# Kernel tuning notes

Hardware: AMD Instinct MI355X
Metric: run time of the kernel (lower is better)

The kernel has to match this reference:

```python
import jax, jax.numpy as jnp
import numpy as np
from jax.scipy.special import logsumexp

ITERS = 50
EPS = 0.005
B, N, D = 8, 2048, 3


def _sq_cost(x, y):
    x2 = jnp.sum(x * x, axis=-1)  # [B,N]
    y2 = jnp.sum(y * y, axis=-1)  # [B,M]
    c = x2[:, :, None] + y2[:, None, :] - 2.0 * jnp.einsum('bnd,bmd->bnm', x, y)
    return jnp.maximum(c, 0.0)


def setup_inputs() -> dict:
    key = jax.random.key(0)
    k1, k2 = jax.random.split(key)
    input1 = jax.random.normal(k1, (B, N, D), dtype=jnp.float32)
    input2 = jax.random.normal(k2, (B, N, D), dtype=jnp.float32)
    return {"input1": input1, "input2": input2}


def reference(input1, input2):
    # Approximate EMD between equal-size point sets, as in emdModule(x, y, eps, iters):
    # iterative entropic-regularized (Sinkhorn/auction-style) assignment on the
    # squared-distance cost, eps = entropic temperature, iters = sweeps.
    eps = jnp.float32(EPS)
    b, n, _ = input1.shape
    m = input2.shape[1]
    C = _sq_cost(input1, input2)  # [B,N,M]
    log_mu = -jnp.log(jnp.float32(n))
    log_nu = -jnp.log(jnp.float32(m))

    def body(carry, _):
        f, g = carry  # duals [B,N], [B,M]
        f = eps * (log_mu - logsumexp((g[:, None, :] - C) / eps, axis=2))
        g = eps * (log_nu - logsumexp((f[:, :, None] - C) / eps, axis=1))
        return (f, g), None

    f0 = jnp.zeros((b, n), dtype=C.dtype)
    g0 = jnp.zeros((b, m), dtype=C.dtype)
    (f, g), _ = jax.lax.scan(body, (f0, g0), None, length=ITERS)

    # transport plan; each row sums to 1/N (soft assignment)
    P = jnp.exp((f[:, :, None] + g[:, None, :] - C) / eps)  # [B,N,M]
    # per-point assigned squared distance (dis of emdModule), then .mean()
    dis = jnp.sum(P * C, axis=-1) * jnp.float32(n)  # [B,N]
    return jnp.mean(dis)
```

## Files before the change

kernel.cpp:

```cpp
#include <hip/hip_runtime.h>
#include <math.h>

#define NB 8
#define NN 2048
#define NM 2048
#define NITERS 50

static constexpr float F_EPS  = 0.005f;
static constexpr float LOG2E  = 1.4426950408889634f;
static constexpr float KK     = LOG2E / F_EPS;
static constexpr float TWOK   = 2.0f * KK;
static constexpr float NEG_LOG2N = -11.0f;

__device__ __forceinline__ float fexp2(float x) { return __builtin_amdgcn_exp2f(x); }
__device__ __forceinline__ float flog2(float x) { return __builtin_amdgcn_logf(x); }

__global__ void pack_init(const float* __restrict__ V, float4* __restrict__ Pout, int total)
{
    int i = blockIdx.x * blockDim.x + threadIdx.x;
    if (i < total) {
        float v0 = V[3*i], v1 = V[3*i+1], v2 = V[3*i+2];
        float s  = fmaf(v0, v0, fmaf(v1, v1, v2*v2));
        Pout[i]  = make_float4(v0, v1, v2, -KK * s);
    }
}

__global__ __launch_bounds__(256, 4) void sink_update(
    const float4* __restrict__ Pin,
    const float*  __restrict__ Vraw,
    float4*       __restrict__ Pout)
{
    __shared__ float2 part [16][257];
    __shared__ float2 part2[16][17];
    const int tid  = threadIdx.x;
    const int lane = tid & 63;
    const int wave = tid >> 6;
    const int wgs_per_b = NN / 16;
    const int b       = blockIdx.x / wgs_per_b;
    const int rowbase = (blockIdx.x % wgs_per_b) * 16;

    float xs0[16], xs1[16], xs2[16];
    {
        const float* vb = Vraw + ((size_t)(b * NN + rowbase)) * 3;
        #pragma unroll
        for (int r = 0; r < 16; ++r) {
            xs0[r] = TWOK * vb[r*3+0];
            xs1[r] = TWOK * vb[r*3+1];
            xs2[r] = TWOK * vb[r*3+2];
        }
    }

    const float4* __restrict__ pp = Pin + b * NM + wave * 512 + lane;

    float rm[16], rs[16];
    #pragma unroll
    for (int r = 0; r < 16; ++r) { rm[r] = -1e30f; rs[r] = 0.f; }

    #pragma unroll
    for (int ib = 0; ib < 2; ++ib) {
        const float4 c0 = pp[(ib*4 + 0) * 64];
        const float4 c1 = pp[(ib*4 + 1) * 64];
        const float4 c2 = pp[(ib*4 + 2) * 64];
        const float4 c3 = pp[(ib*4 + 3) * 64];
        #pragma unroll
        for (int r = 0; r < 16; ++r) {
            const float z0 = fmaf(xs0[r], c0.x, fmaf(xs1[r], c0.y, fmaf(xs2[r], c0.z, c0.w)));
            const float z1 = fmaf(xs0[r], c1.x, fmaf(xs1[r], c1.y, fmaf(xs2[r], c1.z, c1.w)));
            const float z2 = fmaf(xs0[r], c2.x, fmaf(xs1[r], c2.y, fmaf(xs2[r], c2.z, c2.w)));
            const float z3 = fmaf(xs0[r], c3.x, fmaf(xs1[r], c3.y, fmaf(xs2[r], c3.z, c3.w)));
            const float cm = fmaxf(fmaxf(z0, z1), fmaxf(z2, z3));
            const float nm = fmaxf(rm[r], cm);
            const float s  = (fexp2(z0 - nm) + fexp2(z1 - nm))
                           + (fexp2(z2 - nm) + fexp2(z3 - nm));
            rs[r] = fmaf(rs[r], fexp2(rm[r] - nm), s);
            rm[r] = nm;
        }
    }

    #pragma unroll
    for (int r = 0; r < 16; ++r)
        part[r][tid] = make_float2(rm[r], rs[r]);
    __syncthreads();

    {
        const int row = tid & 15, seg = tid >> 4;
        float m16 = -1e30f;
        float2 v[16];
        #pragma unroll
        for (int k = 0; k < 16; ++k) { v[k] = part[row][seg*16 + k]; m16 = fmaxf(m16, v[k].x); }
        float s16 = 0.f;
        #pragma unroll
        for (int k = 0; k < 16; ++k) s16 = fmaf(v[k].y, fexp2(v[k].x - m16), s16);
        part2[row][seg] = make_float2(m16, s16);
    }
    __syncthreads();

    if (tid < 16) {
        float gm = -1e30f;
        float2 v[16];
        #pragma unroll
        for (int k = 0; k < 16; ++k) { v[k] = part2[tid][k]; gm = fmaxf(gm, v[k].x); }
        float s = 0.f;
        #pragma unroll
        for (int k = 0; k < 16; ++k) s = fmaf(v[k].y, fexp2(v[k].x - gm), s);
        const float lse2 = gm + flog2(s);
        const int n0 = rowbase + tid;
        const float* vp = Vraw + ((size_t)(b * NN + n0)) * 3;
        Pout[b * NN + n0] = make_float4(vp[0], vp[1], vp[2], NEG_LOG2N - lse2);
    }
}

__global__ __launch_bounds__(256, 4) void final_loss(
    const float4* __restrict__ Px, const float4* __restrict__ Py,
    float* __restrict__ out)
{
    __shared__ float wsum[4];
    const int tid  = threadIdx.x;
    const int lane = tid & 63;
    const int wave = tid >> 6;
    const int wgs_per_b = NN / 16;
    const int b       = blockIdx.x / wgs_per_b;
    const int rowbase = (blockIdx.x % wgs_per_b) * 16;

    float xr0[16], xr1[16], xr2[16], Af[16], xq[16];
    {
        const float4* xb = Px + b * NN + rowbase;
        #pragma unroll
        for (int r = 0; r < 16; ++r) {
            const float4 xp = xb[r];
            xr0[r] = xp.x; xr1[r] = xp.y; xr2[r] = xp.z; Af[r] = xp.w;
            xq[r]  = fmaf(xp.x, xp.x, fmaf(xp.y, xp.y, xp.z * xp.z));
        }
    }

    const float4* __restrict__ pp = Py + b * NM + wave * 512 + lane;

    float acc = 0.f;
    #pragma unroll
    for (int i = 0; i < 8; ++i) {
        const float4 p = pp[i * 64];
        const float ysq = fmaf(p.x, p.x, fmaf(p.y, p.y, p.z * p.z));
        #pragma unroll
        for (int r = 0; r < 16; ++r) {
            const float dot = fmaf(xr0[r], p.x, fmaf(xr1[r], p.y, xr2[r] * p.z));
            const float cc  = fmaxf(fmaf(-2.f, dot, xq[r] + ysq), 0.f);
            const float zp  = fmaf(TWOK, dot, Af[r] + p.w);
            acc = fmaf(fexp2(zp), cc, acc);
        }
    }
    #pragma unroll
    for (int o = 32; o > 0; o >>= 1) acc += __shfl_xor(acc, o);
    if (lane == 0) wsum[wave] = acc;
    __syncthreads();
    if (tid == 0) {
        atomicAdd(out, (wsum[0] + wsum[1] + wsum[2] + wsum[3]) * (1.0f / NB));
    }
}

extern "C" void kernel_launch(void* const* d_in, const int* in_sizes, int n_in,
                              void* d_out, int out_size, void* d_ws, size_t ws_size,
                              hipStream_t stream)
{
    const float* x = (const float*)d_in[0];
    const float* y = (const float*)d_in[1];
    float4* Px = (float4*)d_ws;
    float4* Py = Px + NB * NN;

    pack_init<<<(NB * NM + 255) / 256, 256, 0, stream>>>(y, Py, NB * NM);

    for (int it = 0; it < NITERS; ++it) {
        sink_update<<<NB * NN / 16, 256, 0, stream>>>(Py, x, Px);
        sink_update<<<NB * NM / 16, 256, 0, stream>>>(Px, y, Py);
    }

    hipMemsetAsync(d_out, 0, sizeof(float), stream);
    final_loss<<<NB * NN / 16, 256, 0, stream>>>(Px, Py, (float*)d_out);
}
```

Baseline: 1.121 ms.

## Use SoA layout, two-pass max-then-sum logsumexp with wave-skip, packed FMA

Converts the point and dual storage from AoS float4 to SoA arrays so each lane loads four consecutive columns with vector loads and uses packed 2-wide FMAs. The online logsumexp becomes two passes: first the row max, then exp-sums. A wave-uniform skip bypasses exp work when every lane's values are more than 28 log2 units below the max. The final loss likewise skips terms whose exponent is below -40. It also interleaves batches across blocks. The costs are recomputing the dot products twice and a small approximation from the skipped tiny terms.

Result: slower. 2.406 ms (+114.6%).

```diff
diff --git a/kernel.cpp b/kernel.cpp
--- a/kernel.cpp
+++ b/kernel.cpp
@@ -6,80 +6,130 @@
 #define NM 2048
 #define NITERS 50
 
-static constexpr float F_EPS  = 0.005f;
 static constexpr float LOG2E  = 1.4426950408889634f;
-static constexpr float KK     = LOG2E / F_EPS;
+static constexpr float KK     = LOG2E / 0.005f;
 static constexpr float TWOK   = 2.0f * KK;
 static constexpr float NEG_LOG2N = -11.0f;
+static constexpr float SKIP   = 28.0f;
+static constexpr float ZP_CUT = -40.0f;
+
+typedef float v2f __attribute__((ext_vector_type(2)));
 
 __device__ __forceinline__ float fexp2(float x) { return __builtin_amdgcn_exp2f(x); }
 __device__ __forceinline__ float flog2(float x) { return __builtin_amdgcn_logf(x); }
-
-__global__ void pack_init(const float* __restrict__ V, float4* __restrict__ Pout, int total)
+__device__ __forceinline__ v2f fma2(float s, v2f a, v2f b) {
+    return __builtin_elementwise_fma((v2f){s, s}, a, b);
+}
+__device__ __forceinline__ v2f vfma2(v2f a, v2f b, v2f c) {
+    return __builtin_elementwise_fma(a, b, c);
+}
+__device__ __forceinline__ v2f max2(v2f a, v2f b) { return __builtin_elementwise_max(a, b); }
+
+__global__ void pack_soa(const float* __restrict__ X, const float* __restrict__ Y,
+                         float* __restrict__ Xx, float* __restrict__ Xy, float* __restrict__ Xz,
+                         float* __restrict__ Yx, float* __restrict__ Yy, float* __restrict__ Yz,
+                         float* __restrict__ SwY)
 {
     int i = blockIdx.x * blockDim.x + threadIdx.x;
-    if (i < total) {
-        float v0 = V[3*i], v1 = V[3*i+1], v2 = V[3*i+2];
-        float s  = fmaf(v0, v0, fmaf(v1, v1, v2*v2));
-        Pout[i]  = make_float4(v0, v1, v2, -KK * s);
+    if (i < NB * NN) {
+        float a = X[3*i], b = X[3*i+1], c = X[3*i+2];
+        Xx[i] = a; Xy[i] = b; Xz[i] = c;
+        float d = Y[3*i], e = Y[3*i+1], f = Y[3*i+2];
+        Yx[i] = d; Yy[i] = e; Yz[i] = f;
+        SwY[i] = -KK * fmaf(d, d, fmaf(e, e, f * f));
     }
 }
 
 __global__ __launch_bounds__(256, 4) void sink_update(
-    const float4* __restrict__ Pin,
-    const float*  __restrict__ Vraw,
-    float4*       __restrict__ Pout)
+    const float* __restrict__ Ux, const float* __restrict__ Uy,
+    const float* __restrict__ Uz, const float* __restrict__ Uw,
+    const float* __restrict__ Ox, const float* __restrict__ Oy,
+    const float* __restrict__ Oz,
+    float* __restrict__ SwOut)
 {
     __shared__ float2 part [16][257];
     __shared__ float2 part2[16][17];
     const int tid  = threadIdx.x;
     const int lane = tid & 63;
     const int wave = tid >> 6;
-    const int wgs_per_b = NN / 16;
-    const int b       = blockIdx.x / wgs_per_b;
-    const int rowbase = (blockIdx.x % wgs_per_b) * 16;
+    const int b    = blockIdx.x & 7;
+    const int wgb  = blockIdx.x >> 3;
+    const int rowbase = wgb * 16;
 
     float xs0[16], xs1[16], xs2[16];
-    {
-        const float* vb = Vraw + ((size_t)(b * NN + rowbase)) * 3;
+    #pragma unroll
+    for (int r = 0; r < 16; ++r) {
+        const int n = b * NN + rowbase + r;
+        xs0[r] = TWOK * Ox[n]; xs1[r] = TWOK * Oy[n]; xs2[r] = TWOK * Oz[n];
+    }
+
+    const int m0 = b * NM + wave * 512 + lane * 4;
+
+    float rm[16];
+    #pragma unroll
+    for (int r = 0; r < 16; ++r) rm[r] = -1e30f;
+
+    #pragma unroll
+    for (int c = 0; c < 2; ++c) {
+        const int mo = m0 + c * 256;
+        const float4 vx = *(const float4*)(Ux + mo);
+        const float4 vy = *(const float4*)(Uy + mo);
+        const float4 vz = *(const float4*)(Uz + mo);
+        const float4 vw = *(const float4*)(Uw + mo);
+        const v2f xlo = {vx.x, vx.y}, xhi = {vx.z, vx.w};
+        const v2f ylo = {vy.x, vy.y}, yhi = {vy.z, vy.w};
+        const v2f zlo = {vz.x, vz.y}, zhi = {vz.z, vz.w};
+        const v2f wlo = {vw.x, vw.y}, whi = {vw.z, vw.w};
         #pragma unroll
         for (int r = 0; r < 16; ++r) {
-            xs0[r] = TWOK * vb[r*3+0];
-            xs1[r] = TWOK * vb[r*3+1];
-            xs2[r] = TWOK * vb[r*3+2];
+            v2f za = fma2(xs0[r], xlo, wlo);
+            za     = fma2(xs1[r], ylo, za);
+            za     = fma2(xs2[r], zlo, za);
+            v2f zb = fma2(xs0[r], xhi, whi);
+            zb     = fma2(xs1[r], yhi, zb);
+            zb     = fma2(xs2[r], zhi, zb);
+            const v2f mm = max2(za, zb);
+            rm[r] = fmaxf(rm[r], fmaxf(mm.x, mm.y));
         }
     }
 
-    const float4* __restrict__ pp = Pin + b * NM + wave * 512 + lane;
-
-    float rm[16], rs[16];
-    #pragma unroll
-    for (int r = 0; r < 16; ++r) { rm[r] = -1e30f; rs[r] = 0.f; }
-
-    #pragma unroll
-    for (int ib = 0; ib < 2; ++ib) {
-        const float4 c0 = pp[(ib*4 + 0) * 64];
-        const float4 c1 = pp[(ib*4 + 1) * 64];
-        const float4 c2 = pp[(ib*4 + 2) * 64];
-        const float4 c3 = pp[(ib*4 + 3) * 64];
+    float rs[16];
+    #pragma unroll
+    for (int r = 0; r < 16; ++r) rs[r] = 0.f;
+
+    #pragma unroll
+    for (int c = 0; c < 2; ++c) {
+        const int mo = m0 + c * 256;
+        const float4 vx = *(const float4*)(Ux + mo);
+        const float4 vy = *(const float4*)(Uy + mo);
+        const float4 vz = *(const float4*)(Uz + mo);
+        const float4 vw = *(const float4*)(Uw + mo);
+        const v2f xlo = {vx.x, vx.y}, xhi = {vx.z, vx.w};
+        const v2f ylo = {vy.x, vy.y}, yhi = {vy.z, vy.w};
+        const v2f zlo = {vz.x, vz.y}, zhi = {vz.z, vz.w};
+        const v2f wlo = {vw.x, vw.y}, whi = {vw.z, vw.w};
         #pragma unroll
         for (int r = 0; r < 16; ++r) {
-            const float z0 = fmaf(xs0[r], c0.x, fmaf(xs1[r], c0.y, fmaf(xs2[r], c0.z, c0.w)));
-            const float z1 = fmaf(xs0[r], c1.x, fmaf(xs1[r], c1.y, fmaf(xs2[r], c1.z, c1.w)));
-            const float z2 = fmaf(xs0[r], c2.x, fmaf(xs1[r], c2.y, fmaf(xs2[r], c2.z, c2.w)));
-            const float z3 = fmaf(xs0[r], c3.x, fmaf(xs1[r], c3.y, fmaf(xs2[r], c3.z, c3.w)));
-            const float cm = fmaxf(fmaxf(z0, z1), fmaxf(z2, z3));
-            const float nm = fmaxf(rm[r], cm);
-            const float s  = (fexp2(z0 - nm) + fexp2(z1 - nm))
-                           + (fexp2(z2 - nm) + fexp2(z3 - nm));
-            rs[r] = fmaf(rs[r], fexp2(rm[r] - nm), s);
-            rm[r] = nm;
+            v2f za = fma2(xs0[r], xlo, wlo);
+            za     = fma2(xs1[r], ylo, za);
+            za     = fma2(xs2[r], zlo, za);
+            v2f zb = fma2(xs0[r], xhi, whi);
+            zb     = fma2(xs1[r], yhi, zb);
+            zb     = fma2(xs2[r], zhi, zb);
+            const v2f mm = max2(za, zb);
+            const float cm = fmaxf(mm.x, mm.y);
+            if (__any(cm > rm[r] - SKIP)) {
+                const float e0 = fexp2(za.x - rm[r]);
+                const float e1 = fexp2(za.y - rm[r]);
+                const float e2 = fexp2(zb.x - rm[r]);
+                const float e3 = fexp2(zb.y - rm[r]);
+                rs[r] += (e0 + e1) + (e2 + e3);
+            }
         }
     }
 
     #pragma unroll
-    for (int r = 0; r < 16; ++r)
-        part[r][tid] = make_float2(rm[r], rs[r]);
+    for (int r = 0; r < 16; ++r) part[r][tid] = make_float2(rm[r], rs[r]);
     __syncthreads();
 
     {
@@ -104,57 +154,77 @@
         #pragma unroll
         for (int k = 0; k < 16; ++k) s = fmaf(v[k].y, fexp2(v[k].x - gm), s);
         const float lse2 = gm + flog2(s);
-        const int n0 = rowbase + tid;
-        const float* vp = Vraw + ((size_t)(b * NN + n0)) * 3;
-        Pout[b * NN + n0] = make_float4(vp[0], vp[1], vp[2], NEG_LOG2N - lse2);
+        SwOut[b * NN + rowbase + tid] = NEG_LOG2N - lse2;
     }
 }
 
 __global__ __launch_bounds__(256, 4) void final_loss(
-    const float4* __restrict__ Px, const float4* __restrict__ Py,
+    const float* __restrict__ Xx, const float* __restrict__ Xy,
+    const float* __restrict__ Xz, const float* __restrict__ SwX,
+    const float* __restrict__ Yx, const float* __restrict__ Yy,
+    const float* __restrict__ Yz, const float* __restrict__ SwY,
     float* __restrict__ out)
 {
     __shared__ float wsum[4];
     const int tid  = threadIdx.x;
     const int lane = tid & 63;
     const int wave = tid >> 6;
-    const int wgs_per_b = NN / 16;
-    const int b       = blockIdx.x / wgs_per_b;
-    const int rowbase = (blockIdx.x % wgs_per_b) * 16;
-
-    float xr0[16], xr1[16], xr2[16], Af[16], xq[16];
-    {
-        const float4* xb = Px + b * NN + rowbase;
+    const int b    = blockIdx.x & 7;
+    const int wgb  = blockIdx.x >> 3;
+    const int rowbase = wgb * 16;
+
+    float px[16], py[16], pz[16], Af[16], xq[16];
+    #pragma unroll
+    for (int r = 0; r < 16; ++r) {
+        const int n = b * NN + rowbase + r;
+        px[r] = Xx[n]; py[r] = Xy[n]; pz[r] = Xz[n];
+        Af[r] = SwX[n];
+        xq[r] = fmaf(px[r], px[r], fmaf(py[r], py[r], pz[r] * pz[r]));
+    }
+
+    const int m0 = b * NM + wave * 512 + lane * 4;
+
+    float acc = 0.f;
+    #pragma unroll
+    for (int c = 0; c < 2; ++c) {
+        const int mo = m0 + c * 256;
+        const float4 vx = *(const float4*)(Yx + mo);
+        const float4 vy = *(const float4*)(Yy + mo);
+        const float4 vz = *(const float4*)(Yz + mo);
+        const float4 vw = *(const float4*)(SwY + mo);
+        const v2f xlo = {vx.x, vx.y}, xhi = {vx.z, vx.w};
+        const v2f ylo = {vy.x, vy.y}, yhi = {vy.z, vy.w};
+        const v2f zlo = {vz.x, vz.y}, zhi = {vz.z, vz.w};
+        const v2f wlo = {vw.x, vw.y}, whi = {vw.z, vw.w};
+        const v2f yqlo = vfma2(xlo, xlo, vfma2(ylo, ylo, zlo * zlo));
+        const v2f yqhi = vfma2(xhi, xhi, vfma2(yhi, yhi, zhi * zhi));
         #pragma unroll
         for (int r = 0; r < 16; ++r) {
-            const float4 xp = xb[r];
-            xr0[r] = xp.x; xr1[r] = xp.y; xr2[r] = xp.z; Af[r] = xp.w;
-            xq[r]  = fmaf(xp.x, xp.x, fmaf(xp.y, xp.y, xp.z * xp.z));
-        }
-    }
-
-    const float4* __restrict__ pp = Py + b * NM + wave * 512 + lane;
-
-    float acc = 0.f;
-    #pragma unroll
-    for (int i = 0; i < 8; ++i) {
-        const float4 p = pp[i * 64];
-        const float ysq = fmaf(p.x, p.x, fmaf(p.y, p.y, p.z * p.z));
-        #pragma unroll
-        for (int r = 0; r < 16; ++r) {
-            const float dot = fmaf(xr0[r], p.x, fmaf(xr1[r], p.y, xr2[r] * p.z));
-            const float cc  = fmaxf(fmaf(-2.f, dot, xq[r] + ysq), 0.f);
-            const float zp  = fmaf(TWOK, dot, Af[r] + p.w);
-            acc = fmaf(fexp2(zp), cc, acc);
+            v2f dlo = fma2(px[r], xlo, fma2(py[r], ylo, (v2f){pz[r], pz[r]} * zlo));
+            v2f dhi = fma2(px[r], xhi, fma2(py[r], yhi, (v2f){pz[r], pz[r]} * zhi));
+            const v2f afb = {Af[r], Af[r]};
+            const v2f zplo = fma2(TWOK, dlo, wlo + afb);
+            const v2f zphi = fma2(TWOK, dhi, whi + afb);
+            const v2f mm = max2(zplo, zphi);
+            if (__any(fmaxf(mm.x, mm.y) > ZP_CUT)) {
+                const v2f xqb = {xq[r], xq[r]};
+                v2f cclo = fma2(-2.f, dlo, yqlo + xqb);
+                v2f cchi = fma2(-2.f, dhi, yqhi + xqb);
+                cclo = max2(cclo, (v2f){0.f, 0.f});
+                cchi = max2(cchi, (v2f){0.f, 0.f});
+                acc = fmaf(fexp2(zplo.x), cclo.x, acc);
+                acc = fmaf(fexp2(zplo.y), cclo.y, acc);
+                acc = fmaf(fexp2(zphi.x), cchi.x, acc);
+                acc = fmaf(fexp2(zphi.y), cchi.y, acc);
+            }
         }
     }
     #pragma unroll
     for (int o = 32; o > 0; o >>= 1) acc += __shfl_xor(acc, o);
     if (lane == 0) wsum[wave] = acc;
     __syncthreads();
-    if (tid == 0) {
+    if (tid == 0)
         atomicAdd(out, (wsum[0] + wsum[1] + wsum[2] + wsum[3]) * (1.0f / NB));
-    }
 }
 
 extern "C" void kernel_launch(void* const* d_in, const int* in_sizes, int n_in,
@@ -163,16 +233,20 @@
 {
     const float* x = (const float*)d_in[0];
     const float* y = (const float*)d_in[1];
-    float4* Px = (float4*)d_ws;
-    float4* Py = Px + NB * NN;
-
-    pack_init<<<(NB * NM + 255) / 256, 256, 0, stream>>>(y, Py, NB * NM);
+    float* w = (float*)d_ws;
+    const int NP = NB * NN;
+    float* Xx = w;          float* Xy = w + NP;     float* Xz = w + 2*NP;
+    float* SwX = w + 3*NP;
+    float* Yx = w + 4*NP;   float* Yy = w + 5*NP;   float* Yz = w + 6*NP;
+    float* SwY = w + 7*NP;
+
+    pack_soa<<<(NP + 255) / 256, 256, 0, stream>>>(x, y, Xx, Xy, Xz, Yx, Yy, Yz, SwY);
 
     for (int it = 0; it < NITERS; ++it) {
-        sink_update<<<NB * NN / 16, 256, 0, stream>>>(Py, x, Px);
-        sink_update<<<NB * NM / 16, 256, 0, stream>>>(Px, y, Py);
+        sink_update<<<NP / 16, 256, 0, stream>>>(Yx, Yy, Yz, SwY, Xx, Xy, Xz, SwX);
+        sink_update<<<NP / 16, 256, 0, stream>>>(Xx, Xy, Xz, SwX, Yx, Yy, Yz, SwY);
     }
 
     hipMemsetAsync(d_out, 0, sizeof(float), stream);
-    final_loss<<<NB * NN / 16, 256, 0, stream>>>(Px, Py, (float*)d_out);
-}
+    final_loss<<<NP / 16, 256, 0, stream>>>(Xx, Xy, Xz, SwX, Yx, Yy, Yz, SwY, (float*)d_out);
+}
```
